# Kernel tuning notes

Measured on AMD Instinct MI355X. Metric: run time of the kernel, lower is better.

Reference implementation:

```python
import jax, jax.numpy as jnp
import numpy as np

B, S, IN_D, OUT_D, QD = 4, 1024, 16, 16, 32
HID, HEADS, HD, L, TED = 256, 8, 32, 4, 256
DECAY = 0.1
SCALE = HD ** -0.5


def _ln(x):
    m = x.mean(-1, keepdims=True)
    v = ((x - m) ** 2).mean(-1, keepdims=True)
    return (x - m) * jax.lax.rsqrt(v + 1e-5)


def _lin(x, w, b):
    # torch nn.Linear: y = x @ W^T + b, W is [out, in]
    return jnp.einsum('...i,oi->...o', x, w) + b


def _sin_emb(t, dim):
    half = dim // 2
    freqs = jnp.exp(-np.log(10000.0) * jnp.arange(half, dtype=jnp.float32) / (half - 1))
    a = t[:, None] * freqs[None, :]
    return jnp.concatenate([jnp.sin(a), jnp.cos(a)], axis=-1)


def _mish(x):
    return x * jnp.tanh(jax.nn.softplus(x))


def _gelu(x):
    return jax.nn.gelu(x, approximate=False)


def setup_inputs() -> dict:
    key = jax.random.key(0)
    ks = iter(jax.random.split(key, 64))

    def w(shape):
        return jax.random.normal(next(ks), shape, dtype=jnp.float32) * 0.02

    d = {}
    d['x'] = jax.random.normal(next(ks), (B, S, IN_D), dtype=jnp.float32)
    d['query'] = jax.random.normal(next(ks), (B, QD), dtype=jnp.float32)
    d['time'] = jax.random.uniform(next(ks), (B,), dtype=jnp.float32) * 1000.0
    d['tm_w1'] = w((TED * 4, TED)); d['tm_b1'] = jnp.zeros((TED * 4,), jnp.float32)
    d['tm_w2'] = w((TED, TED * 4)); d['tm_b2'] = jnp.zeros((TED,), jnp.float32)
    d['in_w'] = w((HID, IN_D)); d['in_b'] = jnp.zeros((HID,), jnp.float32)
    d['q_w1'] = w((HID, QD)); d['q_b1'] = jnp.zeros((HID,), jnp.float32)
    d['q_w2'] = w((HID, HID)); d['q_b2'] = jnp.zeros((HID,), jnp.float32)
    d['n1_w'] = jnp.ones((L, HID), jnp.float32); d['n1_b'] = jnp.zeros((L, HID), jnp.float32)
    d['qkv_w'] = w((L, 3 * HID, HID)); d['qkv_b'] = jnp.zeros((L, 3 * HID), jnp.float32)
    d['ap_w'] = w((L, HID, HID)); d['ap_b'] = jnp.zeros((L, HID), jnp.float32)
    d['rel_bias'] = w((L, 2 * S - 1, HEADS))
    d['n2_w'] = jnp.ones((L, HID), jnp.float32); d['n2_b'] = jnp.zeros((L, HID), jnp.float32)
    d['f1_w'] = w((L, 4 * HID, HID)); d['f1_b'] = jnp.zeros((L, 4 * HID), jnp.float32)
    d['f2_w'] = w((L, HID, 4 * HID)); d['f2_b'] = jnp.zeros((L, HID), jnp.float32)
    d['t1_w'] = w((L, HID, TED)); d['t1_b'] = jnp.zeros((L, HID), jnp.float32)
    d['t2_w'] = w((L, HID, HID)); d['t2_b'] = jnp.zeros((L, HID), jnp.float32)
    d['out_w'] = w((OUT_D, HID)); d['out_b'] = jnp.zeros((OUT_D,), jnp.float32)
    return d


def reference(x, query, time, tm_w1, tm_b1, tm_w2, tm_b2, in_w, in_b,
              q_w1, q_b1, q_w2, q_b2, n1_w, n1_b, qkv_w, qkv_b, ap_w, ap_b,
              rel_bias, n2_w, n2_b, f1_w, f1_b, f2_w, f2_b, t1_w, t1_b,
              t2_w, t2_b, out_w, out_b):
    Bx, Sx, _ = x.shape
    # time MLP: SinusoidalPosEmb -> Linear -> Mish -> Linear
    te = _lin(_sin_emb(time, TED), tm_w1, tm_b1)
    te = _lin(_mish(te), tm_w2, tm_b2)            # [B, TED]
    # input projection + query conditioning (relative-pos path: no abs pos emb)
    h = _lin(x, in_w, in_b)                        # [B, S, HID]
    qe = _lin(_gelu(_lin(query, q_w1, q_b1)), q_w2, q_b2)
    h = h + qe[:, None, :]
    # shared relative-distance structures
    idx = jnp.arange(Sx)
    rel = idx[:, None] - idx[None, :]              # [S, S]
    dec = jnp.exp(-DECAY * jnp.abs(rel).astype(jnp.float32))
    rel_idx = rel + S - 1                          # index into 2*max_seq_len-1 table
    for l in range(L):
        # time conditioning per block
        tp = _lin(_gelu(_lin(te, t1_w[l], t1_b[l])), t2_w[l], t2_b[l])
        xn = _ln(h + tp[:, None, :]) * n1_w[l] + n1_b[l]
        qkv = _lin(xn, qkv_w[l], qkv_b[l]).reshape(Bx, Sx, 3, HEADS, HD)
        qkv = qkv.transpose(2, 0, 3, 1, 4)          # [3, B, H, S, hd]
        q_, k_, v_ = qkv[0], qkv[1], qkv[2]
        attn = jnp.einsum('bhqd,bhkd->bhqk', q_, k_) * SCALE
        bias = rel_bias[l][rel_idx]                 # [S, S, H]
        attn = attn + (dec[:, :, None] * bias).transpose(2, 0, 1)[None]
        a = jax.nn.softmax(attn, axis=-1)
        o = jnp.einsum('bhqk,bhkd->bhqd', a, v_)
        o = o.transpose(0, 2, 1, 3).reshape(Bx, Sx, HID)
        h = h + _lin(o, ap_w[l], ap_b[l])           # residual from pre-time x
        xn2 = _ln(h) * n2_w[l] + n2_b[l]
        h = h + _lin(_gelu(_lin(xn2, f1_w[l], f1_b[l])), f2_w[l], f2_b[l])
    return _lin(h, out_w, out_b)
```

## Files before the change

### kernel.cpp

```cpp
#include <hip/hip_runtime.h>
#include <hip/hip_bf16.h>
#include <math.h>

#define S_LEN 1024
#define HID 256
#define HEADS 8
#define HD 32
#define NLAYER 4
#define TED 256
#define BATCH 4
#define DECAY 0.1f
#define ATT_SCALE 0.17677669529663687f
#define LOG2E 1.4426950408889634f

typedef __bf16 bf8_t __attribute__((ext_vector_type(8)));
typedef float f4_t __attribute__((ext_vector_type(4)));

__device__ __forceinline__ float gelu_f(float x) {
  return 0.5f * x * (1.f + erff(x * 0.70710678118654752f));
}
__device__ __forceinline__ __bf16 f2bf(float f) { return (__bf16)f; }

__global__ __launch_bounds__(256) void k_boot(
    const float* __restrict__ s0, __bf16* __restrict__ d0,
    const float* __restrict__ s1, __bf16* __restrict__ d1,
    const float* __restrict__ s2, __bf16* __restrict__ d2,
    const float* __restrict__ s3, __bf16* __restrict__ d3,
    const float* __restrict__ relb, float* __restrict__ decb_t,
    const float* __restrict__ timev,
    const float* __restrict__ tm_w1, const float* __restrict__ tm_b1,
    const float* __restrict__ query,
    const float* __restrict__ q_w1, const float* __restrict__ q_b1,
    float* __restrict__ te1, float* __restrict__ q1) {
  int bid = blockIdx.x;
  int lane = threadIdx.x & 63;
  if (bid < 1536) {
    const float* s; __bf16* d; int base;
    if (bid < 384)       { s = s0; d = d0; base = bid; }
    else if (bid < 512)  { s = s1; d = d1; base = bid - 384; }
    else if (bid < 1024) { s = s2; d = d2; base = bid - 512; }
    else                 { s = s3; d = d3; base = bid - 1024; }
    int i = (base * 256 + threadIdx.x) * 8;
    float4 a = *(const float4*)(s + i);
    float4 b = *(const float4*)(s + i + 4);
    bf8_t o;
    o[0] = f2bf(a.x); o[1] = f2bf(a.y); o[2] = f2bf(a.z); o[3] = f2bf(a.w);
    o[4] = f2bf(b.x); o[5] = f2bf(b.y); o[6] = f2bf(b.z); o[7] = f2bf(b.w);
    *(bf8_t*)(d + i) = o;
  } else if (bid < 1792) {
    int lb = bid - 1536;
    int l = lb >> 6;
    int i = (lb & 63) * 256 + threadIdx.x;
    if (i < 2047 * 8) {
      int idx = i >> 3, hh = i & 7;
      float dec = __expf(-DECAY * fabsf((float)(idx - 1023)));
      decb_t[(l * 8 + hh) * 2048 + idx] = dec * relb[(size_t)l * 2047 * 8 + i] * LOG2E;
    }
  } else if (bid < 2816) {
    int r = (bid - 1792) * 4 + (threadIdx.x >> 6);
    int o = r & 1023, b = r >> 10;
    float t = timev[b];
    float ev[4];
#pragma unroll
    for (int e = 0; e < 4; e++) {
      int k = lane * 4 + e;
      int i = k & 127;
      float f = __expf(-logf(10000.f) * (float)i / 127.f);
      float a = t * f;
      ev[e] = (k < 128) ? sinf(a) : cosf(a);
    }
    float4 w4 = *(const float4*)(tm_w1 + (size_t)o * 256 + lane * 4);
    float s = ev[0] * w4.x + ev[1] * w4.y + ev[2] * w4.z + ev[3] * w4.w;
#pragma unroll
    for (int off = 32; off; off >>= 1) s += __shfl_xor(s, off);
    if (lane == 0) {
      s += tm_b1[o];
      float sp = (s > 20.f) ? s : log1pf(__expf(s));
      te1[r] = s * tanhf(sp);
    }
  } else {
    int r = (bid - 2816) * 4 + (threadIdx.x >> 6);
    int o = r & 255, b = r >> 8;
    float s = 0.f;
    if (lane < 8) {
      float4 a4 = *(const float4*)(query + b * 32 + lane * 4);
      float4 w4 = *(const float4*)(q_w1 + (size_t)o * 32 + lane * 4);
      s = a4.x * w4.x + a4.y * w4.y + a4.z * w4.z + a4.w * w4.w;
    }
#pragma unroll
    for (int off = 32; off; off >>= 1) s += __shfl_xor(s, off);
    if (lane == 0) q1[r] = gelu_f(s + q_b1[o]);
  }
}

__global__ __launch_bounds__(256) void k_prep_b(
    const float* __restrict__ te1, const float* __restrict__ tm_w2,
    const float* __restrict__ tm_b2,
    const float* __restrict__ q1, const float* __restrict__ q_w2,
    const float* __restrict__ q_b2,
    float* __restrict__ te, float* __restrict__ qe) {
  int bid = blockIdx.x;
  int lane = threadIdx.x & 63;
  bool iste = bid < 256;
  int r = (iste ? bid : bid - 256) * 4 + (threadIdx.x >> 6);
  int o = r & 255, b = r >> 8;
  int K = iste ? 1024 : 256;
  const float* a = (iste ? te1 : q1) + (size_t)b * K;
  const float* w = (iste ? tm_w2 : q_w2) + (size_t)o * K;
  float s = 0.f;
  for (int k = lane * 4; k < K; k += 256) {
    float4 a4 = *(const float4*)(a + k);
    float4 w4 = *(const float4*)(w + k);
    s += a4.x * w4.x + a4.y * w4.y + a4.z * w4.z + a4.w * w4.w;
  }
#pragma unroll
  for (int off = 32; off; off >>= 1) s += __shfl_xor(s, off);
  if (lane == 0) {
    s += (iste ? tm_b2 : q_b2)[o];
    (iste ? te : qe)[r] = s;
  }
}

__global__ __launch_bounds__(256) void k_mid(
    const float* __restrict__ te, const float* __restrict__ t1_w,
    const float* __restrict__ t1_b, float* __restrict__ tt,
    const float* __restrict__ x, const float* __restrict__ in_w,
    const float* __restrict__ in_b, const float* __restrict__ qe,
    float* __restrict__ h) {
  int bid = blockIdx.x;
  if (bid < 1024) {
    int r = bid * 4 + (threadIdx.x >> 6);
    int lane = threadIdx.x & 63;
    int o = r & 255;
    int b = (r >> 8) & 3;
    int g = r >> 10;
    const float* a = te + (size_t)b * 256;
    const float* w = t1_w + ((size_t)(g * 256 + o)) * 256;
    float s = 0.f;
    for (int k = lane * 4; k < 256; k += 256) {
      float4 a4 = *(const float4*)(a + k);
      float4 w4 = *(const float4*)(w + k);
      s += a4.x * w4.x + a4.y * w4.y + a4.z * w4.z + a4.w * w4.w;
    }
#pragma unroll
    for (int off = 32; off; off >>= 1) s += __shfl_xor(s, off);
    if (lane == 0) tt[r] = gelu_f(s + t1_b[g * 256 + o]);
  } else {
    int row = bid - 1024;
    int b = row >> 10;
    int j = threadIdx.x;
    __shared__ float xr[16];
    if (j < 16) xr[j] = x[row * 16 + j];
    __syncthreads();
    float s = in_b[j] + qe[b * 256 + j];
    const float* w = in_w + j * 16;
#pragma unroll
    for (int i = 0; i < 16; i++) s += xr[i] * w[i];
    h[(size_t)row * 256 + j] = s;
  }
}

template <int ACT, bool APG>
__global__ __launch_bounds__(256) void k_gemv(
    const float* __restrict__ A, const float* __restrict__ W,
    const float* __restrict__ bias, float* __restrict__ out,
    int K, int OUT) {
  int r = blockIdx.x * 4 + (threadIdx.x >> 6);
  int lane = threadIdx.x & 63;
  int o = r % OUT;
  int b = (r / OUT) % BATCH;
  int g = r / (OUT * BATCH);
  const float* a = A + (size_t)((APG ? g * BATCH : 0) + b) * K;
  const float* w = W + (size_t)(g * OUT + o) * K;
  float s = 0.f;
  for (int k = lane * 4; k < K; k += 256) {
    float4 a4 = *(const float4*)(a + k);
    float4 w4 = *(const float4*)(w + k);
    s += a4.x * w4.x + a4.y * w4.y + a4.z * w4.z + a4.w * w4.w;
  }
#pragma unroll
  for (int off = 32; off; off >>= 1) s += __shfl_xor(s, off);
  if (lane == 0) {
    s += bias[g * OUT + o];
    if (ACT == 1) s = gelu_f(s);
    if (ACT == 2) {
      float sp = (s > 20.f) ? s : log1pf(__expf(s));
      s = s * tanhf(sp);
    }
    out[r] = s;
  }
}

template <int BN, int ACT, int OUTMODE, bool HASTP>
__global__ __launch_bounds__(256) void k_gemm_lnf(
    const float* __restrict__ h, const __bf16* __restrict__ W,
    const float* __restrict__ bias, void* __restrict__ Cv,
    const float* __restrict__ tp, const float* __restrict__ lw,
    const float* __restrict__ lb, int N) {
  constexpr int K = 256;
  constexpr int NJ = (BN / 2) / 16;
  constexpr int BQ = BN / 64;
  __shared__ __bf16 Al[64 * 264];
  __shared__ __bf16 Bl[2 * BN * 32];
  int tid = threadIdx.x;
  int w = tid >> 6, lane = tid & 63;
  int g = lane >> 4, c = lane & 15;
  int n0 = blockIdx.x * BN, m0 = blockIdx.y * 64;

  int srow = tid >> 2;
  int scol = (tid & 3) * 8;
  int sw = (((tid & 3) ^ ((tid >> 3) & 3))) * 8;
  const __bf16* Wb = W + (size_t)n0 * K + scol;
  bf8_t nB[2][BQ];
#pragma unroll
  for (int sub = 0; sub < 2; sub++)
#pragma unroll
    for (int q = 0; q < BQ; q++)
      nB[sub][q] = *(const bf8_t*)(Wb + (size_t)(q * 64 + srow) * K + sub * 32);

  int sub32 = tid & 31, lrow = tid >> 5;
  int colb = sub32 * 8;
  float4 lw0 = *(const float4*)(lw + colb), lw1 = *(const float4*)(lw + colb + 4);
  float4 lb0 = *(const float4*)(lb + colb), lb1 = *(const float4*)(lb + colb + 4);
  float4 tp0, tp1;
  if (HASTP) {
    const float* tpr = tp + (m0 >> 10) * 256 + colb;
    tp0 = *(const float4*)tpr; tp1 = *(const float4*)(tpr + 4);
  }
#pragma unroll
  for (int p = 0; p < 8; p++) {
    int row = p * 8 + lrow;
    const float* hr = h + (size_t)(m0 + row) * 256 + colb;
    float4 a = *(const float4*)hr;
    float4 b2 = *(const float4*)(hr + 4);
    if (HASTP) {
      a.x += tp0.x; a.y += tp0.y; a.z += tp0.z; a.w += tp0.w;
      b2.x += tp1.x; b2.y += tp1.y; b2.z += tp1.z; b2.w += tp1.w;
    }
    float sum = a.x + a.y + a.z + a.w + b2.x + b2.y + b2.z + b2.w;
    float ss = a.x * a.x + a.y * a.y + a.z * a.z + a.w * a.w +
               b2.x * b2.x + b2.y * b2.y + b2.z * b2.z + b2.w * b2.w;
#pragma unroll
    for (int m = 1; m < 32; m <<= 1) {
      sum += __shfl_xor(sum, m);
      ss += __shfl_xor(ss, m);
    }
    float mean = sum * (1.f / 256.f);
    float var = ss * (1.f / 256.f) - mean * mean;
    float rs = rsqrtf(var + 1e-5f);
    bf8_t o;
    o[0] = f2bf((a.x - mean) * rs * lw0.x + lb0.x);
    o[1] = f2bf((a.y - mean) * rs * lw0.y + lb0.y);
    o[2] = f2bf((a.z - mean) * rs * lw0.z + lb0.z);
    o[3] = f2bf((a.w - mean) * rs * lw0.w + lb0.w);
    o[4] = f2bf((b2.x - mean) * rs * lw1.x + lb1.x);
    o[5] = f2bf((b2.y - mean) * rs * lw1.y + lb1.y);
    o[6] = f2bf((b2.z - mean) * rs * lw1.z + lb1.z);
    o[7] = f2bf((b2.w - mean) * rs * lw1.w + lb1.w);
    *(bf8_t*)&Al[row * 264 + colb] = o;
  }

  int wr = (w >> 1) * 32, wc = (w & 1) * (BN / 2);
  int aseg = ((g ^ ((c >> 1) & 3))) * 8;
  f4_t acc[2][NJ];
#pragma unroll
  for (int i = 0; i < 2; i++)
#pragma unroll
    for (int j = 0; j < NJ; j++) acc[i][j] = (f4_t){0.f, 0.f, 0.f, 0.f};

#pragma unroll
  for (int ph = 0; ph < 4; ph++) {
    __syncthreads();
#pragma unroll
    for (int sub = 0; sub < 2; sub++)
#pragma unroll
      for (int q = 0; q < BQ; q++)
        *(bf8_t*)&Bl[sub * BN * 32 + (q * 64 + srow) * 32 + sw] = nB[sub][q];
    __syncthreads();
    if (ph < 3) {
#pragma unroll
      for (int sub = 0; sub < 2; sub++)
#pragma unroll
        for (int q = 0; q < BQ; q++)
          nB[sub][q] = *(const bf8_t*)(Wb + (size_t)(q * 64 + srow) * K +
                                       (ph + 1) * 64 + sub * 32);
    }
#pragma unroll
    for (int sub = 0; sub < 2; sub++) {
      bf8_t af[2], bfr[NJ];
#pragma unroll
      for (int i = 0; i < 2; i++)
        af[i] = *(const bf8_t*)&Al[(wr + i * 16 + c) * 264 + ph * 64 + sub * 32 + g * 8];
#pragma unroll
      for (int j = 0; j < NJ; j++)
        bfr[j] = *(const bf8_t*)&Bl[sub * BN * 32 + (wc + j * 16 + c) * 32 + aseg];
#pragma unroll
      for (int i = 0; i < 2; i++)
#pragma unroll
        for (int j = 0; j < NJ; j++)
          acc[i][j] = __builtin_amdgcn_mfma_f32_16x16x32_bf16(af[i], bfr[j], acc[i][j], 0, 0, 0);
    }
  }
#pragma unroll
  for (int j = 0; j < NJ; j++) {
    int col = n0 + wc + j * 16 + c;
    float bv = bias[col];
#pragma unroll
    for (int i = 0; i < 2; i++) {
#pragma unroll
      for (int rr = 0; rr < 4; rr++) {
        int row = m0 + wr + i * 16 + 4 * g + rr;
        float v = acc[i][j][rr] + bv;
        if (ACT == 1) v = gelu_f(v);
        size_t idx = (size_t)row * N + col;
        if (OUTMODE == 1) ((float*)Cv)[idx] += v;
        else ((__bf16*)Cv)[idx] = f2bf(v);
      }
    }
  }
}

__global__ __launch_bounds__(256) void k_attn(
    const __bf16* __restrict__ qkv, const float* __restrict__ decb_t,
    __bf16* __restrict__ obuf) {
  __shared__ __bf16 Kl[128 * 40];
  __shared__ __bf16 Vt[32 * 136];
  __shared__ __bf16 Pl[4][16 * 136];
  __shared__ float db[1088];

  int tid = threadIdx.x;
  int w = tid >> 6, lane = tid & 63;
  int g = lane >> 4, c = lane & 15;
  int bh = blockIdx.y;
  int b = bh >> 3, hh = bh & 7;
  int q0 = blockIdx.x * 64;

  for (int i = tid; i < 1087; i += 256) db[i] = decb_t[hh * 2048 + q0 + i];

  bf8_t qraw = *(const bf8_t*)(qkv + ((size_t)(b * S_LEN + q0 + w * 16 + c)) * 768 + hh * 32 + 8 * g);
  bf8_t qfrag;
#pragma unroll
  for (int i = 0; i < 8; i++) qfrag[i] = f2bf((float)qraw[i] * (ATT_SCALE * LOG2E));

  float ps_acc[4] = {0.f, 0.f, 0.f, 0.f};
  f4_t o0 = {0.f, 0.f, 0.f, 0.f}, o1 = {0.f, 0.f, 0.f, 0.f};

  int rowb = w * 16 + 4 * g;
  __bf16* Plw = &Pl[w][0];

  int kvr = tid & 127;
  int part = tid >> 7;
  const __bf16* base0 = qkv + ((size_t)(b * S_LEN + kvr)) * 768 + hh * 32 + part * 16;
  bf8_t k8a = *(const bf8_t*)(base0 + 256);
  bf8_t k8b = *(const bf8_t*)(base0 + 264);
  bf8_t v8a = *(const bf8_t*)(base0 + 512);
  bf8_t v8b = *(const bf8_t*)(base0 + 520);

  for (int c0 = 0; c0 < S_LEN; c0 += 128) {
    __syncthreads();
    {
      *(bf8_t*)&Kl[kvr * 40 + part * 16] = k8a;
      *(bf8_t*)&Kl[kvr * 40 + part * 16 + 8] = k8b;
      int d0s = part * 16;
#pragma unroll
      for (int jj = 0; jj < 8; jj++) Vt[(d0s + jj) * 136 + kvr] = v8a[jj];
#pragma unroll
      for (int jj = 0; jj < 8; jj++) Vt[(d0s + 8 + jj) * 136 + kvr] = v8b[jj];
    }
    __syncthreads();
    if (c0 + 128 < S_LEN) {
      const __bf16* basen = base0 + (size_t)(c0 + 128) * 768;
      k8a = *(const bf8_t*)(basen + 256);
      k8b = *(const bf8_t*)(basen + 264);
      v8a = *(const bf8_t*)(basen + 512);
      v8b = *(const bf8_t*)(basen + 520);
    }

    f4_t sc[8];
    f4_t zero4 = {0.f, 0.f, 0.f, 0.f};
    __builtin_amdgcn_s_setprio(1);
#pragma unroll
    for (int j = 0; j < 8; j++) {
      bf8_t kfrag = *(const bf8_t*)&Kl[(j * 16 + c) * 40 + g * 8];
      sc[j] = __builtin_amdgcn_mfma_f32_16x16x32_bf16(qfrag, kfrag, zero4, 0, 0, 0);
    }
    __builtin_amdgcn_s_setprio(0);
#pragma unroll
    for (int j = 0; j < 8; j++) {
      int bidx = rowb + 1023 - (c0 + j * 16 + c);
#pragma unroll
      for (int r = 0; r < 4; r++) {
        float p = exp2f(sc[j][r] + db[bidx + r]);
        ps_acc[r] += p;
        Plw[(4 * g + r) * 136 + j * 16 + c] = f2bf(p);
      }
    }
    __builtin_amdgcn_s_setprio(1);
#pragma unroll
    for (int ss = 0; ss < 4; ss++) {
      bf8_t pa = *(const bf8_t*)&Plw[c * 136 + ss * 32 + g * 8];
      bf8_t v0 = *(const bf8_t*)&Vt[c * 136 + ss * 32 + g * 8];
      bf8_t v1 = *(const bf8_t*)&Vt[(c + 16) * 136 + ss * 32 + g * 8];
      o0 = __builtin_amdgcn_mfma_f32_16x16x32_bf16(pa, v0, o0, 0, 0, 0);
      o1 = __builtin_amdgcn_mfma_f32_16x16x32_bf16(pa, v1, o1, 0, 0, 0);
    }
    __builtin_amdgcn_s_setprio(0);
  }

#pragma unroll
  for (int r = 0; r < 4; r++) {
#pragma unroll
    for (int m = 1; m < 16; m <<= 1) ps_acc[r] += __shfl_xor(ps_acc[r], m);
    float inv = 1.f / ps_acc[r];
    size_t rowg = (size_t)(b * S_LEN + q0 + rowb + r);
    obuf[rowg * 256 + hh * 32 + c] = f2bf(o0[r] * inv);
    obuf[rowg * 256 + hh * 32 + 16 + c] = f2bf(o1[r] * inv);
  }
}

__global__ __launch_bounds__(512) void k_back(
    const __bf16* __restrict__ obb, float* __restrict__ h,
    const __bf16* __restrict__ wap, const float* __restrict__ apb,
    const float* __restrict__ n2w, const float* __restrict__ n2b,
    const __bf16* __restrict__ wf1, const float* __restrict__ f1b,
    const __bf16* __restrict__ wf2, const float* __restrict__ f2b) {
  __shared__ __bf16 Asm[16 * 264];
  __shared__ __bf16 Bl[2 * 256 * 32];
  __shared__ __bf16 y1l[16 * 1032];
  __shared__ float red[16][8][2];

  int tid = threadIdx.x;
  int w = tid >> 6, lane = tid & 63;
  int g = lane >> 4, c = lane & 15;
  int m0 = blockIdx.x * 16;
  int srow = tid >> 2;
  int scol = (tid & 3) * 8;
  int sw = (((tid & 3) ^ ((srow >> 1) & 3))) * 8;
  int wc = w * 32;
  int axor = (c >> 1) & 3;
  int boff0 = (wc + c) * 32 + ((g ^ axor)) * 8;
  int boff1 = (wc + 16 + c) * 32 + ((g ^ axor)) * 8;
  int col0 = wc + c, col1 = wc + 16 + c;
  f4_t zero4 = {0.f, 0.f, 0.f, 0.f};

  bf8_t nB[2][2];
  auto prefetch = [&](const __bf16* base, int K, int ko) {
#pragma unroll
    for (int s = 0; s < 2; s++)
#pragma unroll
      for (int q = 0; q < 2; q++)
        nB[s][q] = *(const bf8_t*)(base + (size_t)(q * 128 + srow) * K + ko + s * 32 + scol);
  };
  auto stageB = [&]() {
    __syncthreads();
#pragma unroll
    for (int s = 0; s < 2; s++)
#pragma unroll
      for (int q = 0; q < 2; q++)
        *(bf8_t*)&Bl[s * 8192 + (q * 128 + srow) * 32 + sw] = nB[s][q];
    __syncthreads();
  };
  f4_t a0, a1;
  auto mstep = [&](const __bf16* Ab, int AS, int ko) {
#pragma unroll
    for (int s = 0; s < 2; s++) {
      bf8_t af = *(const bf8_t*)&Ab[c * AS + ko + s * 32 + g * 8];
      bf8_t b0 = *(const bf8_t*)&Bl[s * 8192 + boff0];
      bf8_t b1 = *(const bf8_t*)&Bl[s * 8192 + boff1];
      a0 = __builtin_amdgcn_mfma_f32_16x16x32_bf16(af, b0, a0, 0, 0, 0);
      a1 = __builtin_amdgcn_mfma_f32_16x16x32_bf16(af, b1, a1, 0, 0, 0);
    }
  };

  prefetch(wap, 256, 0);
  {
    int row = tid >> 5, gr = tid & 31;
    *(bf8_t*)&Asm[row * 264 + gr * 8] = *(const bf8_t*)(obb + (size_t)(m0 + row) * 256 + gr * 8);
  }

  a0 = zero4; a1 = zero4;
#pragma unroll
  for (int ph = 0; ph < 4; ph++) {
    stageB();
    if (ph < 3) prefetch(wap, 256, (ph + 1) * 64);
    else prefetch(wf1, 256, 0);
    mstep(Asm, 264, ph * 64);
  }

  float hn[2][4];
  {
    float b0v = apb[col0], b1v = apb[col1];
    float ps[4], pq[4];
#pragma unroll
    for (int r = 0; r < 4; r++) {
      size_t row = (size_t)(m0 + 4 * g + r);
      float v0 = a0[r] + b0v + h[row * 256 + col0];
      float v1 = a1[r] + b1v + h[row * 256 + col1];
      h[row * 256 + col0] = v0;
      h[row * 256 + col1] = v1;
      hn[0][r] = v0; hn[1][r] = v1;
      ps[r] = v0 + v1;
      pq[r] = v0 * v0 + v1 * v1;
    }
#pragma unroll
    for (int r = 0; r < 4; r++) {
#pragma unroll
      for (int m = 1; m < 16; m <<= 1) {
        ps[r] += __shfl_xor(ps[r], m);
        pq[r] += __shfl_xor(pq[r], m);
      }
    }
    if (c == 0) {
#pragma unroll
      for (int r = 0; r < 4; r++) {
        red[4 * g + r][w][0] = ps[r];
        red[4 * g + r][w][1] = pq[r];
      }
    }
  }
  __syncthreads();
  {
    float n2w0 = n2w[col0], n2b0 = n2b[col0];
    float n2w1 = n2w[col1], n2b1 = n2b[col1];
#pragma unroll
    for (int r = 0; r < 4; r++) {
      int row = 4 * g + r;
      float S = 0.f, Q = 0.f;
#pragma unroll
      for (int ww = 0; ww < 8; ww++) { S += red[row][ww][0]; Q += red[row][ww][1]; }
      float mean = S * (1.f / 256.f);
      float var = Q * (1.f / 256.f) - mean * mean;
      float rs = rsqrtf(var + 1e-5f);
      Asm[row * 264 + col0] = f2bf((hn[0][r] - mean) * rs * n2w0 + n2b0);
      Asm[row * 264 + col1] = f2bf((hn[1][r] - mean) * rs * n2w1 + n2b1);
    }
  }

#pragma unroll
  for (int nc = 0; nc < 4; nc++) {
    a0 = zero4; a1 = zero4;
#pragma unroll
    for (int ph = 0; ph < 4; ph++) {
      stageB();
      if (ph < 3) prefetch(wf1 + nc * 65536, 256, (ph + 1) * 64);
      else if (nc < 3) prefetch(wf1 + (nc + 1) * 65536, 256, 0);
      else prefetch(wf2, 1024, 0);
      mstep(Asm, 264, ph * 64);
    }
    float b0v = f1b[nc * 256 + col0], b1v = f1b[nc * 256 + col1];
#pragma unroll
    for (int r = 0; r < 4; r++) {
      y1l[(4 * g + r) * 1032 + nc * 256 + col0] = f2bf(gelu_f(a0[r] + b0v));
      y1l[(4 * g + r) * 1032 + nc * 256 + col1] = f2bf(gelu_f(a1[r] + b1v));
    }
  }

  a0 = zero4; a1 = zero4;
#pragma unroll
  for (int ph = 0; ph < 16; ph++) {
    stageB();
    if (ph < 15) prefetch(wf2, 1024, (ph + 1) * 64);
    mstep(y1l, 1032, ph * 64);
  }
  {
    float b0v = f2b[col0], b1v = f2b[col1];
#pragma unroll
    for (int r = 0; r < 4; r++) {
      size_t row = (size_t)(m0 + 4 * g + r);
      h[row * 256 + col0] += a0[r] + b0v;
      h[row * 256 + col1] += a1[r] + b1v;
    }
  }
}

__global__ __launch_bounds__(256) void k_out(
    const float* __restrict__ hbuf, const float* __restrict__ out_w,
    const float* __restrict__ out_b, float* __restrict__ out) {
  int tid = threadIdx.x;
  int r = blockIdx.x * 16 + (tid >> 4);
  int c = tid & 15;
  const float4* hr = (const float4*)(hbuf + (size_t)r * 256);
  const float4* w4 = (const float4*)(out_w + c * 256);
  float s = out_b[c];
#pragma unroll 8
  for (int k = 0; k < 64; k++) {
    float4 a = hr[k], b = w4[k];
    s += a.x * b.x + a.y * b.y + a.z * b.z + a.w * b.w;
  }
  out[r * 16 + c] = s;
}

extern "C" void kernel_launch(void* const* d_in, const int* in_sizes, int n_in,
                              void* d_out, int out_size, void* d_ws, size_t ws_size,
                              hipStream_t stream) {
  const float* x      = (const float*)d_in[0];
  const float* query  = (const float*)d_in[1];
  const float* timev  = (const float*)d_in[2];
  const float* tm_w1  = (const float*)d_in[3];
  const float* tm_b1  = (const float*)d_in[4];
  const float* tm_w2  = (const float*)d_in[5];
  const float* tm_b2  = (const float*)d_in[6];
  const float* in_w   = (const float*)d_in[7];
  const float* in_b   = (const float*)d_in[8];
  const float* q_w1   = (const float*)d_in[9];
  const float* q_b1   = (const float*)d_in[10];
  const float* q_w2   = (const float*)d_in[11];
  const float* q_b2   = (const float*)d_in[12];
  const float* n1_w   = (const float*)d_in[13];
  const float* n1_b   = (const float*)d_in[14];
  const float* qkv_w  = (const float*)d_in[15];
  const float* qkv_b  = (const float*)d_in[16];
  const float* ap_w   = (const float*)d_in[17];
  const float* ap_b   = (const float*)d_in[18];
  const float* relb   = (const float*)d_in[19];
  const float* n2_w   = (const float*)d_in[20];
  const float* n2_b   = (const float*)d_in[21];
  const float* f1_w   = (const float*)d_in[22];
  const float* f1_b   = (const float*)d_in[23];
  const float* f2_w   = (const float*)d_in[24];
  const float* f2_b   = (const float*)d_in[25];
  const float* t1_w   = (const float*)d_in[26];
  const float* t1_b   = (const float*)d_in[27];
  const float* t2_w   = (const float*)d_in[28];
  const float* t2_b   = (const float*)d_in[29];
  const float* out_w  = (const float*)d_in[30];
  const float* out_b  = (const float*)d_in[31];
  float* out = (float*)d_out;

  float* ws = (float*)d_ws;
  float*  h    = ws;
  __bf16* qkvb = (__bf16*)(ws + 1572864);
  __bf16* obb  = (__bf16*)(ws + 3145728);
  __bf16* wqkv = (__bf16*)(ws + 5767168);
  __bf16* wap  = (__bf16*)(ws + 6160384);
  __bf16* wf1  = (__bf16*)(ws + 6291456);
  __bf16* wf2  = (__bf16*)(ws + 6815744);
  float* decb  = ws + 7340032;
  float* qe    = decb + 65536;
  float* tp    = qe + 1024;
  float* te1   = tp + 4096;
  float* te    = te1 + 4096;
  float* q1    = te + 1024;
  float* tt    = q1 + 1024;

  k_boot<<<3072, 256, 0, stream>>>(qkv_w, wqkv, ap_w, wap, f1_w, wf1, f2_w, wf2,
                                   relb, decb, timev, tm_w1, tm_b1,
                                   query, q_w1, q_b1, te1, q1);
  k_prep_b<<<512, 256, 0, stream>>>(te1, tm_w2, tm_b2, q1, q_w2, q_b2, te, qe);
  k_mid<<<5120, 256, 0, stream>>>(te, t1_w, t1_b, tt, x, in_w, in_b, qe, h);
  k_gemv<0, true><<<1024, 256, 0, stream>>>(tt, t2_w, t2_b, tp, 256, 256);

  for (int l = 0; l < NLAYER; l++) {
    k_gemm_lnf<128, 0, 2, true><<<dim3(6, 64), 256, 0, stream>>>(
        h, wqkv + (size_t)l * 196608, qkv_b + l * 768, qkvb,
        tp + l * 1024, n1_w + l * 256, n1_b + l * 256, 768);
    k_attn<<<dim3(16, 32), 256, 0, stream>>>(qkvb, decb + l * 16384, obb);
    k_back<<<256, 512, 0, stream>>>(
        obb, h, wap + (size_t)l * 65536, ap_b + l * 256,
        n2_w + l * 256, n2_b + l * 256,
        wf1 + (size_t)l * 262144, f1_b + l * 1024,
        wf2 + (size_t)l * 262144, f2_b + l * 256);
  }
  k_out<<<256, 256, 0, stream>>>(h, out_w, out_b, out);
}
```

Baseline: 279.8 us.

## Fuse all stages into one persistent cooperative kernel with grid syncs

```diff
diff --git a/kernel.cpp b/kernel.cpp
--- a/kernel.cpp
+++ b/kernel.cpp
@@ -1,6 +1,9 @@
 #include <hip/hip_runtime.h>
+#include <hip/hip_cooperative_groups.h>
 #include <hip/hip_bf16.h>
 #include <math.h>
+
+namespace cg = cooperative_groups;
 
 #define S_LEN 1024
 #define HID 256
@@ -21,45 +24,45 @@
 }
 __device__ __forceinline__ __bf16 f2bf(float f) { return (__bf16)f; }
 
-__global__ __launch_bounds__(256) void k_boot(
-    const float* __restrict__ s0, __bf16* __restrict__ d0,
-    const float* __restrict__ s1, __bf16* __restrict__ d1,
-    const float* __restrict__ s2, __bf16* __restrict__ d2,
-    const float* __restrict__ s3, __bf16* __restrict__ d3,
-    const float* __restrict__ relb, float* __restrict__ decb_t,
-    const float* __restrict__ timev,
-    const float* __restrict__ tm_w1, const float* __restrict__ tm_b1,
-    const float* __restrict__ query,
-    const float* __restrict__ q_w1, const float* __restrict__ q_b1,
-    float* __restrict__ te1, float* __restrict__ q1) {
-  int bid = blockIdx.x;
-  int lane = threadIdx.x & 63;
-  if (bid < 1536) {
+struct Params {
+  const float *x, *query, *timev, *tm_w1, *tm_b1, *tm_w2, *tm_b2, *in_w, *in_b;
+  const float *q_w1, *q_b1, *q_w2, *q_b2, *n1_w, *n1_b, *qkv_b, *ap_b;
+  const float *relb, *n2_w, *n2_b, *f1_b, *f2_b, *t1_w, *t1_b, *t2_w, *t2_b;
+  const float *out_w, *out_b;
+  const float *qkv_w, *ap_w, *f1_w, *f2_w;
+  float* out;
+  float *h, *decb, *qe, *tp, *te1, *te, *q1, *tt;
+  __bf16 *qkvb, *obb, *wqkv, *wap, *wf1, *wf2;
+};
+
+__device__ void boot_unit(int u, int tid, const Params& p) {
+  int lane = tid & 63;
+  if (u < 1536) {
     const float* s; __bf16* d; int base;
-    if (bid < 384)       { s = s0; d = d0; base = bid; }
-    else if (bid < 512)  { s = s1; d = d1; base = bid - 384; }
-    else if (bid < 1024) { s = s2; d = d2; base = bid - 512; }
-    else                 { s = s3; d = d3; base = bid - 1024; }
-    int i = (base * 256 + threadIdx.x) * 8;
+    if (u < 384)       { s = p.qkv_w; d = p.wqkv; base = u; }
+    else if (u < 512)  { s = p.ap_w;  d = p.wap;  base = u - 384; }
+    else if (u < 1024) { s = p.f1_w;  d = p.wf1;  base = u - 512; }
+    else               { s = p.f2_w;  d = p.wf2;  base = u - 1024; }
+    int i = (base * 256 + tid) * 8;
     float4 a = *(const float4*)(s + i);
     float4 b = *(const float4*)(s + i + 4);
     bf8_t o;
     o[0] = f2bf(a.x); o[1] = f2bf(a.y); o[2] = f2bf(a.z); o[3] = f2bf(a.w);
     o[4] = f2bf(b.x); o[5] = f2bf(b.y); o[6] = f2bf(b.z); o[7] = f2bf(b.w);
     *(bf8_t*)(d + i) = o;
-  } else if (bid < 1792) {
-    int lb = bid - 1536;
+  } else if (u < 1792) {
+    int lb = u - 1536;
     int l = lb >> 6;
-    int i = (lb & 63) * 256 + threadIdx.x;
+    int i = (lb & 63) * 256 + tid;
     if (i < 2047 * 8) {
       int idx = i >> 3, hh = i & 7;
       float dec = __expf(-DECAY * fabsf((float)(idx - 1023)));
-      decb_t[(l * 8 + hh) * 2048 + idx] = dec * relb[(size_t)l * 2047 * 8 + i] * LOG2E;
-    }
-  } else if (bid < 2816) {
-    int r = (bid - 1792) * 4 + (threadIdx.x >> 6);
+      p.decb[(l * 8 + hh) * 2048 + idx] = dec * p.relb[(size_t)l * 2047 * 8 + i] * LOG2E;
+    }
+  } else if (u < 2816) {
+    int r = (u - 1792) * 4 + (tid >> 6);
     int o = r & 1023, b = r >> 10;
-    float t = timev[b];
+    float t = p.timev[b];
     float ev[4];
 #pragma unroll
     for (int e = 0; e < 4; e++) {
@@ -69,44 +72,38 @@
       float a = t * f;
       ev[e] = (k < 128) ? sinf(a) : cosf(a);
     }
-    float4 w4 = *(const float4*)(tm_w1 + (size_t)o * 256 + lane * 4);
+    float4 w4 = *(const float4*)(p.tm_w1 + (size_t)o * 256 + lane * 4);
     float s = ev[0] * w4.x + ev[1] * w4.y + ev[2] * w4.z + ev[3] * w4.w;
 #pragma unroll
     for (int off = 32; off; off >>= 1) s += __shfl_xor(s, off);
     if (lane == 0) {
-      s += tm_b1[o];
+      s += p.tm_b1[o];
       float sp = (s > 20.f) ? s : log1pf(__expf(s));
-      te1[r] = s * tanhf(sp);
+      p.te1[r] = s * tanhf(sp);
     }
   } else {
-    int r = (bid - 2816) * 4 + (threadIdx.x >> 6);
+    int r = (u - 2816) * 4 + (tid >> 6);
     int o = r & 255, b = r >> 8;
     float s = 0.f;
     if (lane < 8) {
-      float4 a4 = *(const float4*)(query + b * 32 + lane * 4);
-      float4 w4 = *(const float4*)(q_w1 + (size_t)o * 32 + lane * 4);
+      float4 a4 = *(const float4*)(p.query + b * 32 + lane * 4);
+      float4 w4 = *(const float4*)(p.q_w1 + (size_t)o * 32 + lane * 4);
       s = a4.x * w4.x + a4.y * w4.y + a4.z * w4.z + a4.w * w4.w;
     }
 #pragma unroll
     for (int off = 32; off; off >>= 1) s += __shfl_xor(s, off);
-    if (lane == 0) q1[r] = gelu_f(s + q_b1[o]);
-  }
-}
-
-__global__ __launch_bounds__(256) void k_prep_b(
-    const float* __restrict__ te1, const float* __restrict__ tm_w2,
-    const float* __restrict__ tm_b2,
-    const float* __restrict__ q1, const float* __restrict__ q_w2,
-    const float* __restrict__ q_b2,
-    float* __restrict__ te, float* __restrict__ qe) {
-  int bid = blockIdx.x;
-  int lane = threadIdx.x & 63;
-  bool iste = bid < 256;
-  int r = (iste ? bid : bid - 256) * 4 + (threadIdx.x >> 6);
+    if (lane == 0) p.q1[r] = gelu_f(s + p.q_b1[o]);
+  }
+}
+
+__device__ void prepb_unit(int u, int tid, const Params& p) {
+  int lane = tid & 63;
+  bool iste = u < 256;
+  int r = (iste ? u : u - 256) * 4 + (tid >> 6);
   int o = r & 255, b = r >> 8;
   int K = iste ? 1024 : 256;
-  const float* a = (iste ? te1 : q1) + (size_t)b * K;
-  const float* w = (iste ? tm_w2 : q_w2) + (size_t)o * K;
+  const float* a = (iste ? p.te1 : p.q1) + (size_t)b * K;
+  const float* w = (iste ? p.tm_w2 : p.q_w2) + (size_t)o * K;
   float s = 0.f;
   for (int k = lane * 4; k < K; k += 256) {
     float4 a4 = *(const float4*)(a + k);
@@ -116,96 +113,58 @@
 #pragma unroll
   for (int off = 32; off; off >>= 1) s += __shfl_xor(s, off);
   if (lane == 0) {
-    s += (iste ? tm_b2 : q_b2)[o];
-    (iste ? te : qe)[r] = s;
-  }
-}
-
-__global__ __launch_bounds__(256) void k_mid(
-    const float* __restrict__ te, const float* __restrict__ t1_w,
-    const float* __restrict__ t1_b, float* __restrict__ tt,
-    const float* __restrict__ x, const float* __restrict__ in_w,
-    const float* __restrict__ in_b, const float* __restrict__ qe,
-    float* __restrict__ h) {
-  int bid = blockIdx.x;
-  if (bid < 1024) {
-    int r = bid * 4 + (threadIdx.x >> 6);
-    int lane = threadIdx.x & 63;
-    int o = r & 255;
-    int b = (r >> 8) & 3;
-    int g = r >> 10;
-    const float* a = te + (size_t)b * 256;
-    const float* w = t1_w + ((size_t)(g * 256 + o)) * 256;
-    float s = 0.f;
-    for (int k = lane * 4; k < 256; k += 256) {
-      float4 a4 = *(const float4*)(a + k);
-      float4 w4 = *(const float4*)(w + k);
-      s += a4.x * w4.x + a4.y * w4.y + a4.z * w4.z + a4.w * w4.w;
-    }
+    s += (iste ? p.tm_b2 : p.q_b2)[o];
+    (iste ? p.te : p.qe)[r] = s;
+  }
+}
+
+__device__ void mid_unit(int u, int tid, const Params& p) {
+  int lane = tid & 63;
+  if (u < 1024) {
+    int r = u * 4 + (tid >> 6);
+    int o = r & 255, b = (r >> 8) & 3, g = r >> 10;
+    float4 a4 = *(const float4*)(p.te + (size_t)b * 256 + lane * 4);
+    float4 w4 = *(const float4*)(p.t1_w + ((size_t)(g * 256 + o)) * 256 + lane * 4);
+    float s = a4.x * w4.x + a4.y * w4.y + a4.z * w4.z + a4.w * w4.w;
 #pragma unroll
     for (int off = 32; off; off >>= 1) s += __shfl_xor(s, off);
-    if (lane == 0) tt[r] = gelu_f(s + t1_b[g * 256 + o]);
+    if (lane == 0) p.tt[r] = gelu_f(s + p.t1_b[g * 256 + o]);
   } else {
-    int row = bid - 1024;
+    int row = u - 1024;
     int b = row >> 10;
-    int j = threadIdx.x;
-    __shared__ float xr[16];
-    if (j < 16) xr[j] = x[row * 16 + j];
-    __syncthreads();
-    float s = in_b[j] + qe[b * 256 + j];
-    const float* w = in_w + j * 16;
-#pragma unroll
-    for (int i = 0; i < 16; i++) s += xr[i] * w[i];
-    h[(size_t)row * 256 + j] = s;
-  }
-}
-
-template <int ACT, bool APG>
-__global__ __launch_bounds__(256) void k_gemv(
-    const float* __restrict__ A, const float* __restrict__ W,
-    const float* __restrict__ bias, float* __restrict__ out,
-    int K, int OUT) {
-  int r = blockIdx.x * 4 + (threadIdx.x >> 6);
-  int lane = threadIdx.x & 63;
-  int o = r % OUT;
-  int b = (r / OUT) % BATCH;
-  int g = r / (OUT * BATCH);
-  const float* a = A + (size_t)((APG ? g * BATCH : 0) + b) * K;
-  const float* w = W + (size_t)(g * OUT + o) * K;
-  float s = 0.f;
-  for (int k = lane * 4; k < K; k += 256) {
-    float4 a4 = *(const float4*)(a + k);
-    float4 w4 = *(const float4*)(w + k);
-    s += a4.x * w4.x + a4.y * w4.y + a4.z * w4.z + a4.w * w4.w;
-  }
+    float xv = (lane < 16) ? p.x[row * 16 + lane] : 0.f;
+    float s = p.in_b[tid] + p.qe[b * 256 + tid];
+    const float* w = p.in_w + tid * 16;
+#pragma unroll
+    for (int i = 0; i < 16; i++) s += __shfl(xv, i) * w[i];
+    p.h[(size_t)row * 256 + tid] = s;
+  }
+}
+
+__device__ void t2_unit(int u, int tid, const Params& p) {
+  int lane = tid & 63;
+  int r = u * 4 + (tid >> 6);
+  int o = r & 255, b = (r >> 8) & 3, g = r >> 10;
+  float4 a4 = *(const float4*)(p.tt + (size_t)(g * 4 + b) * 256 + lane * 4);
+  float4 w4 = *(const float4*)(p.t2_w + (size_t)(g * 256 + o) * 256 + lane * 4);
+  float s = a4.x * w4.x + a4.y * w4.y + a4.z * w4.z + a4.w * w4.w;
 #pragma unroll
   for (int off = 32; off; off >>= 1) s += __shfl_xor(s, off);
-  if (lane == 0) {
-    s += bias[g * OUT + o];
-    if (ACT == 1) s = gelu_f(s);
-    if (ACT == 2) {
-      float sp = (s > 20.f) ? s : log1pf(__expf(s));
-      s = s * tanhf(sp);
-    }
-    out[r] = s;
-  }
-}
-
-template <int BN, int ACT, int OUTMODE, bool HASTP>
-__global__ __launch_bounds__(256) void k_gemm_lnf(
-    const float* __restrict__ h, const __bf16* __restrict__ W,
-    const float* __restrict__ bias, void* __restrict__ Cv,
-    const float* __restrict__ tp, const float* __restrict__ lw,
-    const float* __restrict__ lb, int N) {
-  constexpr int K = 256;
-  constexpr int NJ = (BN / 2) / 16;
-  constexpr int BQ = BN / 64;
-  __shared__ __bf16 Al[64 * 264];
-  __shared__ __bf16 Bl[2 * BN * 32];
-  int tid = threadIdx.x;
+  if (lane == 0) p.tp[r] = s + p.t2_b[g * 256 + o];
+}
+
+__device__ void qkv_phase(int vb, int tid, int l, __bf16* Al, __bf16* Bl,
+                          const Params& p) {
+  constexpr int K = 256, BN = 128, NJ = 4, BQ = 2;
+  const __bf16* W = p.wqkv + (size_t)l * 196608;
+  const float* bias = p.qkv_b + l * 768;
+  const float* tp = p.tp + l * 1024;
+  const float* lw = p.n1_w + l * 256;
+  const float* lb = p.n1_b + l * 256;
+  const int N = 768;
   int w = tid >> 6, lane = tid & 63;
   int g = lane >> 4, c = lane & 15;
-  int n0 = blockIdx.x * BN, m0 = blockIdx.y * 64;
+  int n0 = (vb % 6) * BN, m0 = (vb / 6) * 64;
 
   int srow = tid >> 2;
   int scol = (tid & 3) * 8;
@@ -222,21 +181,16 @@
   int colb = sub32 * 8;
   float4 lw0 = *(const float4*)(lw + colb), lw1 = *(const float4*)(lw + colb + 4);
   float4 lb0 = *(const float4*)(lb + colb), lb1 = *(const float4*)(lb + colb + 4);
-  float4 tp0, tp1;
-  if (HASTP) {
-    const float* tpr = tp + (m0 >> 10) * 256 + colb;
-    tp0 = *(const float4*)tpr; tp1 = *(const float4*)(tpr + 4);
-  }
-#pragma unroll
-  for (int p = 0; p < 8; p++) {
-    int row = p * 8 + lrow;
-    const float* hr = h + (size_t)(m0 + row) * 256 + colb;
+  const float* tpr = tp + (m0 >> 10) * 256 + colb;
+  float4 tp0 = *(const float4*)tpr, tp1 = *(const float4*)(tpr + 4);
+#pragma unroll
+  for (int ph = 0; ph < 8; ph++) {
+    int row = ph * 8 + lrow;
+    const float* hr = p.h + (size_t)(m0 + row) * 256 + colb;
     float4 a = *(const float4*)hr;
     float4 b2 = *(const float4*)(hr + 4);
-    if (HASTP) {
-      a.x += tp0.x; a.y += tp0.y; a.z += tp0.z; a.w += tp0.w;
-      b2.x += tp1.x; b2.y += tp1.y; b2.z += tp1.z; b2.w += tp1.w;
-    }
+    a.x += tp0.x; a.y += tp0.y; a.z += tp0.z; a.w += tp0.w;
+    b2.x += tp1.x; b2.y += tp1.y; b2.z += tp1.z; b2.w += tp1.w;
     float sum = a.x + a.y + a.z + a.w + b2.x + b2.y + b2.z + b2.w;
     float ss = a.x * a.x + a.y * a.y + a.z * a.z + a.w * a.w +
                b2.x * b2.x + b2.y * b2.y + b2.z * b2.z + b2.w * b2.w;
@@ -310,30 +264,25 @@
 #pragma unroll
       for (int rr = 0; rr < 4; rr++) {
         int row = m0 + wr + i * 16 + 4 * g + rr;
-        float v = acc[i][j][rr] + bv;
-        if (ACT == 1) v = gelu_f(v);
-        size_t idx = (size_t)row * N + col;
-        if (OUTMODE == 1) ((float*)Cv)[idx] += v;
-        else ((__bf16*)Cv)[idx] = f2bf(v);
+        p.qkvb[(size_t)row * N + col] = f2bf(acc[i][j][rr] + bv);
       }
     }
   }
 }
 
-__global__ __launch_bounds__(256) void k_attn(
-    const __bf16* __restrict__ qkv, const float* __restrict__ decb_t,
-    __bf16* __restrict__ obuf) {
-  __shared__ __bf16 Kl[128 * 40];
-  __shared__ __bf16 Vt[32 * 136];
-  __shared__ __bf16 Pl[4][16 * 136];
-  __shared__ float db[1088];
-
-  int tid = threadIdx.x;
+__device__ void attn_phase(int vb, int tid, int l, char* smem, const Params& p) {
+  __bf16* Kl = (__bf16*)smem;
+  __bf16* Vt = Kl + 5120;
+  __bf16* Pl = Vt + 4352;
+  float* db = (float*)(smem + 36352);
+  const __bf16* qkv = p.qkvb;
+  const float* decb_t = p.decb + l * 16384;
+
   int w = tid >> 6, lane = tid & 63;
   int g = lane >> 4, c = lane & 15;
-  int bh = blockIdx.y;
+  int bh = vb >> 4;
   int b = bh >> 3, hh = bh & 7;
-  int q0 = blockIdx.x * 64;
+  int q0 = (vb & 15) * 64;
 
   for (int i = tid; i < 1087; i += 256) db[i] = decb_t[hh * 2048 + q0 + i];
 
@@ -346,7 +295,7 @@
   f4_t o0 = {0.f, 0.f, 0.f, 0.f}, o1 = {0.f, 0.f, 0.f, 0.f};
 
   int rowb = w * 16 + 4 * g;
-  __bf16* Plw = &Pl[w][0];
+  __bf16* Plw = Pl + w * 2176;
 
   int kvr = tid & 127;
   int part = tid >> 7;
@@ -390,9 +339,9 @@
       int bidx = rowb + 1023 - (c0 + j * 16 + c);
 #pragma unroll
       for (int r = 0; r < 4; r++) {
-        float p = exp2f(sc[j][r] + db[bidx + r]);
-        ps_acc[r] += p;
-        Plw[(4 * g + r) * 136 + j * 16 + c] = f2bf(p);
+        float pv = exp2f(sc[j][r] + db[bidx + r]);
+        ps_acc[r] += pv;
+        Plw[(4 * g + r) * 136 + j * 16 + c] = f2bf(pv);
       }
     }
     __builtin_amdgcn_s_setprio(1);
@@ -413,26 +362,29 @@
     for (int m = 1; m < 16; m <<= 1) ps_acc[r] += __shfl_xor(ps_acc[r], m);
     float inv = 1.f / ps_acc[r];
     size_t rowg = (size_t)(b * S_LEN + q0 + rowb + r);
-    obuf[rowg * 256 + hh * 32 + c] = f2bf(o0[r] * inv);
-    obuf[rowg * 256 + hh * 32 + 16 + c] = f2bf(o1[r] * inv);
-  }
-}
-
-__global__ __launch_bounds__(512) void k_back(
-    const __bf16* __restrict__ obb, float* __restrict__ h,
-    const __bf16* __restrict__ wap, const float* __restrict__ apb,
-    const float* __restrict__ n2w, const float* __restrict__ n2b,
-    const __bf16* __restrict__ wf1, const float* __restrict__ f1b,
-    const __bf16* __restrict__ wf2, const float* __restrict__ f2b) {
-  __shared__ __bf16 Asm[16 * 264];
-  __shared__ __bf16 Bl[2 * 256 * 32];
-  __shared__ __bf16 y1l[16 * 1032];
-  __shared__ float red[16][8][2];
-
-  int tid = threadIdx.x;
+    p.obb[rowg * 256 + hh * 32 + c] = f2bf(o0[r] * inv);
+    p.obb[rowg * 256 + hh * 32 + 16 + c] = f2bf(o1[r] * inv);
+  }
+}
+
+__device__ void back_phase(int bid, int tid, int l, char* smem, const Params& p) {
+  __bf16* Asm = (__bf16*)smem;
+  __bf16* Bl  = (__bf16*)(smem + 8448);
+  __bf16* y1l = (__bf16*)(smem + 41216);
+  float (*red)[8][2] = (float(*)[8][2])(smem + 74240);
+  const __bf16* wap = p.wap + (size_t)l * 65536;
+  const float* apb = p.ap_b + l * 256;
+  const float* n2w = p.n2_w + l * 256;
+  const float* n2b = p.n2_b + l * 256;
+  const __bf16* wf1 = p.wf1 + (size_t)l * 262144;
+  const float* f1b = p.f1_b + l * 1024;
+  const __bf16* wf2 = p.wf2 + (size_t)l * 262144;
+  const float* f2b = p.f2_b + l * 256;
+  float* h = p.h;
+
   int w = tid >> 6, lane = tid & 63;
   int g = lane >> 4, c = lane & 15;
-  int m0 = blockIdx.x * 16;
+  int m0 = bid * 16;
   int srow = tid >> 2;
   int scol = (tid & 3) * 8;
   int sw = (((tid & 3) ^ ((srow >> 1) & 3))) * 8;
@@ -475,7 +427,7 @@
   prefetch(wap, 256, 0);
   {
     int row = tid >> 5, gr = tid & 31;
-    *(bf8_t*)&Asm[row * 264 + gr * 8] = *(const bf8_t*)(obb + (size_t)(m0 + row) * 256 + gr * 8);
+    *(bf8_t*)&Asm[row * 264 + gr * 8] = *(const bf8_t*)(p.obb + (size_t)(m0 + row) * 256 + gr * 8);
   }
 
   a0 = zero4; a1 = zero4;
@@ -573,93 +525,140 @@
   }
 }
 
-__global__ __launch_bounds__(256) void k_out(
-    const float* __restrict__ hbuf, const float* __restrict__ out_w,
-    const float* __restrict__ out_b, float* __restrict__ out) {
-  int tid = threadIdx.x;
-  int r = blockIdx.x * 16 + (tid >> 4);
+__device__ void out_phase(int bid, int tid, const Params& p) {
+  int r = bid * 16 + (tid >> 4);
   int c = tid & 15;
-  const float4* hr = (const float4*)(hbuf + (size_t)r * 256);
-  const float4* w4 = (const float4*)(out_w + c * 256);
-  float s = out_b[c];
+  const float4* hr = (const float4*)(p.h + (size_t)r * 256);
+  const float4* w4 = (const float4*)(p.out_w + c * 256);
+  float s = p.out_b[c];
 #pragma unroll 8
   for (int k = 0; k < 64; k++) {
     float4 a = hr[k], b = w4[k];
     s += a.x * b.x + a.y * b.y + a.z * b.z + a.w * b.w;
   }
-  out[r * 16 + c] = s;
-}
+  p.out[r * 16 + c] = s;
+}
+
+__global__ __launch_bounds__(512, 2) void k_all(Params p) {
+  cg::grid_group grid = cg::this_grid();
+  __shared__ __align__(16) char smem[100352];
+  int tid512 = threadIdx.x;
+  int vbh = tid512 >> 8;
+  int tid = tid512 & 255;
+  int bid = blockIdx.x;
+  int vb0 = bid * 2 + vbh;
+
+  for (int u = vb0; u < 3072; u += 512) boot_unit(u, tid, p);
+  grid.sync();
+  prepb_unit(vb0, tid, p);
+  grid.sync();
+  for (int u = vb0; u < 5120; u += 512) mid_unit(u, tid, p);
+  grid.sync();
+  for (int u = vb0; u < 1024; u += 512) t2_unit(u, tid, p);
+  grid.sync();
+
+  for (int l = 0; l < NLAYER; l++) {
+    if (vb0 < 384) {
+      qkv_phase(vb0, tid, l, (__bf16*)(smem + vbh * 50176),
+                (__bf16*)(smem + vbh * 50176 + 33792), p);
+    } else {
+#pragma unroll
+      for (int i = 0; i < 8; i++) __syncthreads();
+    }
+    grid.sync();
+    attn_phase(vb0, tid, l, smem + vbh * 40704, p);
+    grid.sync();
+    back_phase(bid, tid512, l, smem, p);
+    grid.sync();
+  }
+  if (tid512 < 256) out_phase(bid, tid512, p);
+}
+
+__global__ __launch_bounds__(256) void kg_boot(Params p) { boot_unit(blockIdx.x, threadIdx.x, p); }
+__global__ __launch_bounds__(256) void kg_prepb(Params p) { prepb_unit(blockIdx.x, threadIdx.x, p); }
+__global__ __launch_bounds__(256) void kg_mid(Params p) { mid_unit(blockIdx.x, threadIdx.x, p); }
+__global__ __launch_bounds__(256) void kg_t2(Params p) { t2_unit(blockIdx.x, threadIdx.x, p); }
+__global__ __launch_bounds__(256) void kg_qkv(Params p, int l) {
+  __shared__ __align__(16) char s[50176];
+  qkv_phase(blockIdx.x, threadIdx.x, l, (__bf16*)s, (__bf16*)(s + 33792), p);
+}
+__global__ __launch_bounds__(256) void kg_attn(Params p, int l) {
+  __shared__ __align__(16) char s[40704];
+  attn_phase(blockIdx.x, threadIdx.x, l, s, p);
+}
+__global__ __launch_bounds__(512) void kg_back(Params p, int l) {
+  __shared__ __align__(16) char s[75264];
+  back_phase(blockIdx.x, threadIdx.x, l, s, p);
+}
+__global__ __launch_bounds__(256) void kg_out(Params p) { out_phase(blockIdx.x, threadIdx.x, p); }
 
 extern "C" void kernel_launch(void* const* d_in, const int* in_sizes, int n_in,
                               void* d_out, int out_size, void* d_ws, size_t ws_size,
                               hipStream_t stream) {
-  const float* x      = (const float*)d_in[0];
-  const float* query  = (const float*)d_in[1];
-  const float* timev  = (const float*)d_in[2];
-  const float* tm_w1  = (const float*)d_in[3];
-  const float* tm_b1  = (const float*)d_in[4];
-  const float* tm_w2  = (const float*)d_in[5];
-  const float* tm_b2  = (const float*)d_in[6];
-  const float* in_w   = (const float*)d_in[7];
-  const float* in_b   = (const float*)d_in[8];
-  const float* q_w1   = (const float*)d_in[9];
-  const float* q_b1   = (const float*)d_in[10];
-  const float* q_w2   = (const float*)d_in[11];
-  const float* q_b2   = (const float*)d_in[12];
-  const float* n1_w   = (const float*)d_in[13];
-  const float* n1_b   = (const float*)d_in[14];
-  const float* qkv_w  = (const float*)d_in[15];
-  const float* qkv_b  = (const float*)d_in[16];
-  const float* ap_w   = (const float*)d_in[17];
-  const float* ap_b   = (const float*)d_in[18];
-  const float* relb   = (const float*)d_in[19];
-  const float* n2_w   = (const float*)d_in[20];
-  const float* n2_b   = (const float*)d_in[21];
-  const float* f1_w   = (const float*)d_in[22];
-  const float* f1_b   = (const float*)d_in[23];
-  const float* f2_w   = (const float*)d_in[24];
-  const float* f2_b   = (const float*)d_in[25];
-  const float* t1_w   = (const float*)d_in[26];
-  const float* t1_b   = (const float*)d_in[27];
-  const float* t2_w   = (const float*)d_in[28];
-  const float* t2_b   = (const float*)d_in[29];
-  const float* out_w  = (const float*)d_in[30];
-  const float* out_b  = (const float*)d_in[31];
-  float* out = (float*)d_out;
+  Params p;
+  p.x      = (const float*)d_in[0];
+  p.query  = (const float*)d_in[1];
+  p.timev  = (const float*)d_in[2];
+  p.tm_w1  = (const float*)d_in[3];
+  p.tm_b1  = (const float*)d_in[4];
+  p.tm_w2  = (const float*)d_in[5];
+  p.tm_b2  = (const float*)d_in[6];
+  p.in_w   = (const float*)d_in[7];
+  p.in_b   = (const float*)d_in[8];
+  p.q_w1   = (const float*)d_in[9];
+  p.q_b1   = (const float*)d_in[10];
+  p.q_w2   = (const float*)d_in[11];
+  p.q_b2   = (const float*)d_in[12];
+  p.n1_w   = (const float*)d_in[13];
+  p.n1_b   = (const float*)d_in[14];
+  p.qkv_w  = (const float*)d_in[15];
+  p.qkv_b  = (const float*)d_in[16];
+  p.ap_w   = (const float*)d_in[17];
+  p.ap_b   = (const float*)d_in[18];
+  p.relb   = (const float*)d_in[19];
+  p.n2_w   = (const float*)d_in[20];
+  p.n2_b   = (const float*)d_in[21];
+  p.f1_w   = (const float*)d_in[22];
+  p.f1_b   = (const float*)d_in[23];
+  p.f2_w   = (const float*)d_in[24];
+  p.f2_b   = (const float*)d_in[25];
+  p.t1_w   = (const float*)d_in[26];
+  p.t1_b   = (const float*)d_in[27];
+  p.t2_w   = (const float*)d_in[28];
+  p.t2_b   = (const float*)d_in[29];
+  p.out_w  = (const float*)d_in[30];
+  p.out_b  = (const float*)d_in[31];
+  p.out = (float*)d_out;
 
   float* ws = (float*)d_ws;
-  float*  h    = ws;
-  __bf16* qkvb = (__bf16*)(ws + 1572864);
-  __bf16* obb  = (__bf16*)(ws + 3145728);
-  __bf16* wqkv = (__bf16*)(ws + 5767168);
-  __bf16* wap  = (__bf16*)(ws + 6160384);
-  __bf16* wf1  = (__bf16*)(ws + 6291456);
-  __bf16* wf2  = (__bf16*)(ws + 6815744);
-  float* decb  = ws + 7340032;
-  float* qe    = decb + 65536;
-  float* tp    = qe + 1024;
-  float* te1   = tp + 4096;
-  float* te    = te1 + 4096;
-  float* q1    = te + 1024;
-  float* tt    = q1 + 1024;
-
-  k_boot<<<3072, 256, 0, stream>>>(qkv_w, wqkv, ap_w, wap, f1_w, wf1, f2_w, wf2,
-                                   relb, decb, timev, tm_w1, tm_b1,
-                                   query, q_w1, q_b1, te1, q1);
-  k_prep_b<<<512, 256, 0, stream>>>(te1, tm_w2, tm_b2, q1, q_w2, q_b2, te, qe);
-  k_mid<<<5120, 256, 0, stream>>>(te, t1_w, t1_b, tt, x, in_w, in_b, qe, h);
-  k_gemv<0, true><<<1024, 256, 0, stream>>>(tt, t2_w, t2_b, tp, 256, 256);
-
-  for (int l = 0; l < NLAYER; l++) {
-    k_gemm_lnf<128, 0, 2, true><<<dim3(6, 64), 256, 0, stream>>>(
-        h, wqkv + (size_t)l * 196608, qkv_b + l * 768, qkvb,
-        tp + l * 1024, n1_w + l * 256, n1_b + l * 256, 768);
-    k_attn<<<dim3(16, 32), 256, 0, stream>>>(qkvb, decb + l * 16384, obb);
-    k_back<<<256, 512, 0, stream>>>(
-        obb, h, wap + (size_t)l * 65536, ap_b + l * 256,
-        n2_w + l * 256, n2_b + l * 256,
-        wf1 + (size_t)l * 262144, f1_b + l * 1024,
-        wf2 + (size_t)l * 262144, f2_b + l * 256);
-  }
-  k_out<<<256, 256, 0, stream>>>(h, out_w, out_b, out);
-}
+  p.h    = ws;
+  p.qkvb = (__bf16*)(ws + 1572864);
+  p.obb  = (__bf16*)(ws + 3145728);
+  p.wqkv = (__bf16*)(ws + 5767168);
+  p.wap  = (__bf16*)(ws + 6160384);
+  p.wf1  = (__bf16*)(ws + 6291456);
+  p.wf2  = (__bf16*)(ws + 6815744);
+  p.decb = ws + 7340032;
+  p.qe   = p.decb + 65536;
+  p.tp   = p.qe + 1024;
+  p.te1  = p.tp + 4096;
+  p.te   = p.te1 + 4096;
+  p.q1   = p.te + 1024;
+  p.tt   = p.q1 + 1024;
+
+  void* args[] = {(void*)&p};
+  hipError_t err = hipLaunchCooperativeKernel((const void*)k_all, dim3(256),
+                                              dim3(512), args, 0, stream);
+  if (err != hipSuccess) {
+    kg_boot<<<3072, 256, 0, stream>>>(p);
+    kg_prepb<<<512, 256, 0, stream>>>(p);
+    kg_mid<<<5120, 256, 0, stream>>>(p);
+    kg_t2<<<1024, 256, 0, stream>>>(p);
+    for (int l = 0; l < NLAYER; l++) {
+      kg_qkv<<<384, 256, 0, stream>>>(p, l);
+      kg_attn<<<512, 256, 0, stream>>>(p, l);
+      kg_back<<<256, 512, 0, stream>>>(p, l);
+    }
+    kg_out<<<256, 256, 0, stream>>>(p);
+  }
+}
```

Result: slower. 754.2 us (+169.5%).
